# Kernel tuning notes

Hardware: AMD Instinct MI355X
Metric: run time of the kernel (lower is better)

The kernel has to match this reference:

```python
import jax, jax.numpy as jnp
import numpy as np

BANDWIDTH = 8.0  # gaussian kernel std


def setup_inputs() -> dict:
    key = jax.random.key(0)
    k1, k2 = jax.random.split(key)
    B, N, M, D = 2, 8192, 8192, 64
    return {
        "points": jax.random.normal(k1, (B, N, D), dtype=jnp.float32),
        "ref_points": jax.random.normal(k2, (B, M, D), dtype=jnp.float32),
    }


def reference(points, ref_points):
    # Squared pairwise distances via the |x|^2 + |y|^2 - 2<x,y> expansion
    # (same math as ((x_i - y_j)**2).sum(-1), avoids a [B,N,M,D] intermediate).
    sq_p = jnp.sum(points * points, axis=-1)          # [B,N]
    sq_r = jnp.sum(ref_points * ref_points, axis=-1)  # [B,M]
    s_ij = (sq_p[:, :, None] + sq_r[:, None, :]
            - 2.0 * jnp.einsum('bnd,bmd->bnm', points, ref_points))  # [B,N,M]
    # Gaussian kernel
    k_ij = jnp.exp(s_ij * (-1.0 / (2.0 * BANDWIDTH ** 2)))  # [B,N,M]
    # Weighted mean of reference points (nominator.sum(2) / k_ij.sum(2))
    nominator = jnp.einsum('bnm,bmd->bnd', k_ij, ref_points)  # [B,N,D]
    denominator = jnp.sum(k_ij, axis=-1, keepdims=True)       # [B,N,1]
    return nominator / denominator
```

## Files before the change

### kernel.cpp

```cpp
#include <hip/hip_runtime.h>

constexpr int B_ = 2, N_ = 8192, M_ = 8192, Dd = 64;
constexpr int TN = 128;
constexpr int TM = 64;
constexpr int SPLIT = 8;
constexpr int MCHUNK = M_ / SPLIT;
constexpr int NCHUNKS = MCHUNK / TM;
constexpr int NT = N_ / TN;
constexpr float LOG2E   = 1.4426950408889634f;
constexpr float SCALE_S = LOG2E / 64.0f;
constexpr float SCALE_N = -LOG2E / 128.0f;

using s16x8 = __attribute__((ext_vector_type(8))) short;
using f32x4 = __attribute__((ext_vector_type(4))) float;

#if defined(__has_builtin)
#if __has_builtin(__builtin_amdgcn_exp2f)
#define EXP2(x) __builtin_amdgcn_exp2f(x)
#endif
#endif
#ifndef EXP2
#define EXP2(x) exp2f(x)
#endif

__device__ __forceinline__ unsigned short f2bf(float f) {
  unsigned u = __builtin_bit_cast(unsigned, f);
  u += 0x7FFFu + ((u >> 16) & 1u);
  return (unsigned short)(u >> 16);
}
__device__ __forceinline__ unsigned pk2(float lo, float hi) {
  return (unsigned)f2bf(lo) | ((unsigned)f2bf(hi) << 16);
}
__device__ __forceinline__ f32x4 mfma16(s16x8 a, s16x8 b, f32x4 c) {
  return __builtin_amdgcn_mfma_f32_16x16x32_bf16(a, b, c, 0, 0, 0);
}


__global__ __launch_bounds__(256, 4) void msflash_kernel(
    const float* __restrict__ pts, const float* __restrict__ ref,
    float* __restrict__ num_acc, float* __restrict__ den_acc) {
  __shared__ unsigned short ldsY [TM][72];
  __shared__ unsigned short ldsYT[Dd][72];
  __shared__ unsigned short ldsP [4][32][72];
  __shared__ float lds_an2[TN];
  __shared__ float lds_bm2[TM];

  const int tid  = threadIdx.x;
  const int w    = tid >> 6;
  const int lane = tid & 63;
  const int l15  = lane & 15, quad = lane >> 4;

  const int s  = blockIdx.x & (SPLIT - 1);
  const int r  = blockIdx.x >> 3;
  const int bb = r / NT;
  const int nt = r % NT;
  const int n0 = nt * TN;
  const int m_begin = s * MCHUNK;

  unsigned short (*ldsX)[72] = (unsigned short (*)[72]) & ldsP[0][0][0];
  {
    const int rowl = tid >> 1, half = tid & 1;
    const float* gp = pts + ((size_t)bb * N_ + n0 + rowl) * Dd + half * 32;
    float sq = 0.f;
    unsigned pkd[16];
#pragma unroll
    for (int i = 0; i < 8; i++) {
      float4 f = ((const float4*)gp)[i];
      sq += f.x * f.x + f.y * f.y + f.z * f.z + f.w * f.w;
      pkd[2 * i + 0] = pk2(f.x, f.y);
      pkd[2 * i + 1] = pk2(f.z, f.w);
    }
    sq += __shfl_xor(sq, 1);
    if (half == 0) lds_an2[rowl] = sq * SCALE_N;
    uint4* dv = (uint4*)&ldsX[rowl][half * 32];
#pragma unroll
    for (int i = 0; i < 4; i++)
      dv[i] = make_uint4(pkd[4 * i], pkd[4 * i + 1], pkd[4 * i + 2], pkd[4 * i + 3]);
  }
  __syncthreads();

  s16x8 bx[2][2];
  float anr_s[2];
#pragma unroll
  for (int rt = 0; rt < 2; rt++) {
#pragma unroll
    for (int ks = 0; ks < 2; ks++)
      bx[rt][ks] = *(const s16x8*)&ldsX[w * 32 + rt * 16 + l15][ks * 32 + quad * 8];
    anr_s[rt] = lds_an2[w * 32 + rt * 16 + l15];
  }

  f32x4 o[2][4], den[2];
#pragma unroll
  for (int rt = 0; rt < 2; rt++) {
    den[rt] = f32x4{0.f, 0.f, 0.f, 0.f};
#pragma unroll
    for (int dt = 0; dt < 4; dt++) o[rt][dt] = f32x4{0.f, 0.f, 0.f, 0.f};
  }
  s16x8 ones;
#pragma unroll
  for (int j = 0; j < 8; j++) ones[j] = (l15 == 0) ? (short)0x3F80 : (short)0;

  for (int c = 0; c < NCHUNKS; c++) {
    __syncthreads();
    {
      const int rowl = tid >> 2, q = tid & 3;
      const float* gp = ref + ((size_t)bb * M_ + m_begin + c * TM + rowl) * Dd + q * 16;
      float sq = 0.f;
      unsigned pkd[8];
#pragma unroll
      for (int i = 0; i < 4; i++) {
        float4 f = ((const float4*)gp)[i];
        sq += f.x * f.x + f.y * f.y + f.z * f.z + f.w * f.w;
        pkd[2 * i + 0] = pk2(f.x, f.y);
        pkd[2 * i + 1] = pk2(f.z, f.w);
      }
      sq += __shfl_xor(sq, 1);
      sq += __shfl_xor(sq, 2);
      if (q == 0) lds_bm2[rowl] = sq * SCALE_N;
      uint4* dv = (uint4*)&ldsY[rowl][q * 16];
      dv[0] = make_uint4(pkd[0], pkd[1], pkd[2], pkd[3]);
      dv[1] = make_uint4(pkd[4], pkd[5], pkd[6], pkd[7]);
#pragma unroll
      for (int j = 0; j < 8; j++) {
        ldsYT[q * 16 + 2 * j + 0][rowl] = (unsigned short)pkd[j];
        ldsYT[q * 16 + 2 * j + 1][rowl] = (unsigned short)(pkd[j] >> 16);
      }
    }
    __syncthreads();

    f32x4 sf[2][4];
#pragma unroll
    for (int ct = 0; ct < 4; ct++) {
      s16x8 a0 = *(const s16x8*)&ldsY[ct * 16 + l15][quad * 8];
      s16x8 a1 = *(const s16x8*)&ldsY[ct * 16 + l15][32 + quad * 8];
#pragma unroll
      for (int rt = 0; rt < 2; rt++) {
        f32x4 acc = f32x4{0.f, 0.f, 0.f, 0.f};
        acc = mfma16(a0, bx[rt][0], acc);
        acc = mfma16(a1, bx[rt][1], acc);
        sf[rt][ct] = acc;
      }
    }
#pragma unroll
    for (int ct = 0; ct < 4; ct++) {
      f32x4 bm = *(const f32x4*)&lds_bm2[ct * 16 + quad * 4];
#pragma unroll
      for (int rt = 0; rt < 2; rt++) {
        float e0 = EXP2(sf[rt][ct][0] * SCALE_S + (anr_s[rt] + bm[0]));
        float e1 = EXP2(sf[rt][ct][1] * SCALE_S + (anr_s[rt] + bm[1]));
        float e2 = EXP2(sf[rt][ct][2] * SCALE_S + (anr_s[rt] + bm[2]));
        float e3 = EXP2(sf[rt][ct][3] * SCALE_S + (anr_s[rt] + bm[3]));
        uint2 w2 = make_uint2(pk2(e0, e1), pk2(e2, e3));
        *(uint2*)&ldsP[w][rt * 16 + l15][ct * 16 + quad * 4] = w2;
      }
    }
    s16x8 pf[2][2];
#pragma unroll
    for (int rt = 0; rt < 2; rt++)
#pragma unroll
      for (int ks = 0; ks < 2; ks++)
        pf[rt][ks] = *(const s16x8*)&ldsP[w][rt * 16 + l15][ks * 32 + quad * 8];
#pragma unroll
    for (int dt = 0; dt < 4; dt++) {
      s16x8 a0 = *(const s16x8*)&ldsYT[dt * 16 + l15][quad * 8];
      s16x8 a1 = *(const s16x8*)&ldsYT[dt * 16 + l15][32 + quad * 8];
#pragma unroll
      for (int rt = 0; rt < 2; rt++) {
        o[rt][dt] = mfma16(a0, pf[rt][0], o[rt][dt]);
        o[rt][dt] = mfma16(a1, pf[rt][1], o[rt][dt]);
      }
    }
#pragma unroll
    for (int rt = 0; rt < 2; rt++) {
      den[rt] = mfma16(ones, pf[rt][0], den[rt]);
      den[rt] = mfma16(ones, pf[rt][1], den[rt]);
    }
  }

  float* ldsO = (float*)&ldsP[w][0][0];
  float* nb = num_acc + ((size_t)bb * N_ + n0) * Dd;
#pragma unroll
  for (int rt = 0; rt < 2; rt++) {
#pragma unroll
    for (int dt = 0; dt < 4; dt++) {
      const int base = l15 * 66 + dt * 16 + quad * 4;
      *(float2*)&ldsO[base + 0] = make_float2(o[rt][dt][0], o[rt][dt][1]);
      *(float2*)&ldsO[base + 2] = make_float2(o[rt][dt][2], o[rt][dt][3]);
    }
    const int nrow = w * 32 + rt * 16;
#pragma unroll
    for (int rr = 0; rr < 16; rr++) {
      float v = ldsO[rr * 66 + lane];
      atomicAdd(&nb[(size_t)(nrow + rr) * Dd + lane], v);
    }
    if (quad == 0)
      atomicAdd(&den_acc[(size_t)bb * N_ + n0 + nrow + l15], den[rt][0]);
  }
}

__global__ __launch_bounds__(256) void msdiv_kernel(
    const float* __restrict__ num, const float* __restrict__ den,
    float* __restrict__ out) {
  const int i = blockIdx.x * 256 + threadIdx.x;
  float4 v = ((const float4*)num)[i];
  const float inv = 1.0f / den[i >> 4];
  ((float4*)out)[i] = make_float4(v.x * inv, v.y * inv, v.z * inv, v.w * inv);
}

extern "C" void kernel_launch(void* const* d_in, const int* in_sizes, int n_in,
                              void* d_out, int out_size, void* d_ws, size_t ws_size,
                              hipStream_t stream) {
  const float* pts = (const float*)d_in[0];
  const float* ref = (const float*)d_in[1];
  float* out = (float*)d_out;
  float* num = (float*)d_ws;
  float* den = num + (size_t)B_ * N_ * Dd;
  const size_t acc_bytes = ((size_t)B_ * N_ * Dd + (size_t)B_ * N_) * sizeof(float);

  hipMemsetAsync(d_ws, 0, acc_bytes, stream);
  msflash_kernel<<<dim3(B_ * NT * SPLIT), dim3(256), 0, stream>>>(pts, ref, num, den);
  const int tot4 = B_ * N_ * Dd / 4;
  msdiv_kernel<<<dim3(tot4 / 256), dim3(256), 0, stream>>>(num, den, out);
}
```

Baseline: 138.4 us.

## Precompute bf16 ref and transpose in prep kernel; read operands directly from global

Adds a prep kernel that converts the reference points to bf16 once, writing row-major and transposed copies plus scaled squared norms to workspace. The main kernel then loads its MFMA operands straight from global memory (L2-cached) instead of reconverting and staging each 64-row chunk into LDS, and drops the two block barriers per chunk. This removes redundant conversion work repeated across every N tile, but adds a kernel launch and extra workspace traffic. It also leaves global-load latency exposed inside the inner loop, with no LDS staging or prefetch to hide it.

```diff
diff --git a/kernel.cpp b/kernel.cpp
--- a/kernel.cpp
+++ b/kernel.cpp
@@ -35,15 +35,56 @@
   return __builtin_amdgcn_mfma_f32_16x16x32_bf16(a, b, c, 0, 0, 0);
 }
 
+__global__ __launch_bounds__(256) void prep_kernel(
+    const float* __restrict__ ref, unsigned short* __restrict__ ybf,
+    unsigned short* __restrict__ ybfT, float* __restrict__ bm2) {
+  __shared__ unsigned short t[64][72];
+  const int bb = blockIdx.x >> 7, mt = blockIdx.x & 127;
+  const int m0 = mt * 64;
+  const int tid = threadIdx.x;
+  {
+    const int rowl = tid >> 2, q = tid & 3;
+    const float* gp = ref + ((size_t)bb * M_ + m0 + rowl) * Dd + q * 16;
+    float sq = 0.f;
+    unsigned pkd[8];
+#pragma unroll
+    for (int i = 0; i < 4; i++) {
+      float4 f = ((const float4*)gp)[i];
+      sq += f.x * f.x + f.y * f.y + f.z * f.z + f.w * f.w;
+      pkd[2 * i + 0] = pk2(f.x, f.y);
+      pkd[2 * i + 1] = pk2(f.z, f.w);
+    }
+    sq += __shfl_xor(sq, 1);
+    sq += __shfl_xor(sq, 2);
+    if (q == 0) bm2[(size_t)bb * M_ + m0 + rowl] = sq * SCALE_N;
+    uint4* gv = (uint4*)(ybf + ((size_t)bb * M_ + m0 + rowl) * Dd + q * 16);
+    gv[0] = make_uint4(pkd[0], pkd[1], pkd[2], pkd[3]);
+    gv[1] = make_uint4(pkd[4], pkd[5], pkd[6], pkd[7]);
+    uint4* tv = (uint4*)&t[rowl][q * 16];
+    tv[0] = make_uint4(pkd[0], pkd[1], pkd[2], pkd[3]);
+    tv[1] = make_uint4(pkd[4], pkd[5], pkd[6], pkd[7]);
+  }
+  __syncthreads();
+  {
+    const int drow = tid >> 2, qm = tid & 3;
+    unsigned po[8];
+#pragma unroll
+    for (int k = 0; k < 8; k++)
+      po[k] = (unsigned)t[qm * 16 + 2 * k][drow] |
+              ((unsigned)t[qm * 16 + 2 * k + 1][drow] << 16);
+    uint4* gv = (uint4*)(ybfT + ((size_t)bb * Dd + drow) * M_ + m0 + qm * 16);
+    gv[0] = make_uint4(po[0], po[1], po[2], po[3]);
+    gv[1] = make_uint4(po[4], po[5], po[6], po[7]);
+  }
+}
+
 
 __global__ __launch_bounds__(256, 4) void msflash_kernel(
-    const float* __restrict__ pts, const float* __restrict__ ref,
+    const float* __restrict__ pts, const unsigned short* __restrict__ ybf,
+    const unsigned short* __restrict__ ybfT, const float* __restrict__ bm2g,
     float* __restrict__ num_acc, float* __restrict__ den_acc) {
-  __shared__ unsigned short ldsY [TM][72];
-  __shared__ unsigned short ldsYT[Dd][72];
   __shared__ unsigned short ldsP [4][32][72];
   __shared__ float lds_an2[TN];
-  __shared__ float lds_bm2[TM];
 
   const int tid  = threadIdx.x;
   const int w    = tid >> 6;
@@ -88,6 +129,7 @@
       bx[rt][ks] = *(const s16x8*)&ldsX[w * 32 + rt * 16 + l15][ks * 32 + quad * 8];
     anr_s[rt] = lds_an2[w * 32 + rt * 16 + l15];
   }
+  __syncthreads();
 
   f32x4 o[2][4], den[2];
 #pragma unroll
@@ -100,39 +142,18 @@
 #pragma unroll
   for (int j = 0; j < 8; j++) ones[j] = (l15 == 0) ? (short)0x3F80 : (short)0;
 
+  const unsigned short* pa = ybf + ((size_t)bb * M_ + m_begin) * Dd;
+  const unsigned short* pt = ybfT + (size_t)bb * Dd * M_ + m_begin;
+  const float* bmg = bm2g + (size_t)bb * M_ + m_begin;
+
   for (int c = 0; c < NCHUNKS; c++) {
-    __syncthreads();
-    {
-      const int rowl = tid >> 2, q = tid & 3;
-      const float* gp = ref + ((size_t)bb * M_ + m_begin + c * TM + rowl) * Dd + q * 16;
-      float sq = 0.f;
-      unsigned pkd[8];
-#pragma unroll
-      for (int i = 0; i < 4; i++) {
-        float4 f = ((const float4*)gp)[i];
-        sq += f.x * f.x + f.y * f.y + f.z * f.z + f.w * f.w;
-        pkd[2 * i + 0] = pk2(f.x, f.y);
-        pkd[2 * i + 1] = pk2(f.z, f.w);
-      }
-      sq += __shfl_xor(sq, 1);
-      sq += __shfl_xor(sq, 2);
-      if (q == 0) lds_bm2[rowl] = sq * SCALE_N;
-      uint4* dv = (uint4*)&ldsY[rowl][q * 16];
-      dv[0] = make_uint4(pkd[0], pkd[1], pkd[2], pkd[3]);
-      dv[1] = make_uint4(pkd[4], pkd[5], pkd[6], pkd[7]);
-#pragma unroll
-      for (int j = 0; j < 8; j++) {
-        ldsYT[q * 16 + 2 * j + 0][rowl] = (unsigned short)pkd[j];
-        ldsYT[q * 16 + 2 * j + 1][rowl] = (unsigned short)(pkd[j] >> 16);
-      }
-    }
-    __syncthreads();
-
+    const int mo = c * TM;
     f32x4 sf[2][4];
 #pragma unroll
     for (int ct = 0; ct < 4; ct++) {
-      s16x8 a0 = *(const s16x8*)&ldsY[ct * 16 + l15][quad * 8];
-      s16x8 a1 = *(const s16x8*)&ldsY[ct * 16 + l15][32 + quad * 8];
+      const unsigned short* row = pa + (size_t)(mo + ct * 16 + l15) * Dd;
+      s16x8 a0 = *(const s16x8*)&row[quad * 8];
+      s16x8 a1 = *(const s16x8*)&row[32 + quad * 8];
 #pragma unroll
       for (int rt = 0; rt < 2; rt++) {
         f32x4 acc = f32x4{0.f, 0.f, 0.f, 0.f};
@@ -143,7 +164,7 @@
     }
 #pragma unroll
     for (int ct = 0; ct < 4; ct++) {
-      f32x4 bm = *(const f32x4*)&lds_bm2[ct * 16 + quad * 4];
+      f32x4 bm = *(const f32x4*)&bmg[mo + ct * 16 + quad * 4];
 #pragma unroll
       for (int rt = 0; rt < 2; rt++) {
         float e0 = EXP2(sf[rt][ct][0] * SCALE_S + (anr_s[rt] + bm[0]));
@@ -162,8 +183,9 @@
         pf[rt][ks] = *(const s16x8*)&ldsP[w][rt * 16 + l15][ks * 32 + quad * 8];
 #pragma unroll
     for (int dt = 0; dt < 4; dt++) {
-      s16x8 a0 = *(const s16x8*)&ldsYT[dt * 16 + l15][quad * 8];
-      s16x8 a1 = *(const s16x8*)&ldsYT[dt * 16 + l15][32 + quad * 8];
+      const unsigned short* trow = pt + (size_t)(dt * 16 + l15) * M_ + mo;
+      s16x8 a0 = *(const s16x8*)&trow[quad * 8];
+      s16x8 a1 = *(const s16x8*)&trow[32 + quad * 8];
 #pragma unroll
       for (int rt = 0; rt < 2; rt++) {
         o[rt][dt] = mfma16(a0, pf[rt][0], o[rt][dt]);
@@ -215,10 +237,15 @@
   float* out = (float*)d_out;
   float* num = (float*)d_ws;
   float* den = num + (size_t)B_ * N_ * Dd;
+  unsigned short* ybf  = (unsigned short*)(den + (size_t)B_ * N_);
+  unsigned short* ybfT = ybf + (size_t)B_ * M_ * Dd;
+  float* bm2 = (float*)(ybfT + (size_t)B_ * M_ * Dd);
   const size_t acc_bytes = ((size_t)B_ * N_ * Dd + (size_t)B_ * N_) * sizeof(float);
 
   hipMemsetAsync(d_ws, 0, acc_bytes, stream);
-  msflash_kernel<<<dim3(B_ * NT * SPLIT), dim3(256), 0, stream>>>(pts, ref, num, den);
+  prep_kernel<<<dim3(B_ * (M_ / 64)), dim3(256), 0, stream>>>(ref, ybf, ybfT, bm2);
+  msflash_kernel<<<dim3(B_ * NT * SPLIT), dim3(256), 0, stream>>>(pts, ybf, ybfT, bm2,
+                                                                  num, den);
   const int tot4 = B_ * N_ * Dd / 4;
   msdiv_kernel<<<dim3(tot4 / 256), dim3(256), 0, stream>>>(num, den, out);
 }
```

Result: slower. 211.8 us (+53.0%).
